# Kernel tuning notes

Measured on AMD Instinct MI355X. Metric: run time of the kernel, lower is better.

## Reference

```python
import itertools
import jax, jax.numpy as jnp
import numpy as np

N_LEVELS = 16
N_FEATS = 2
LOG2_T = 19
BASE_RES = 16.0
FINEST_RES = 512.0
N_POINTS = 2 ** 21
MASK = np.uint32((1 << LOG2_T) - 1)
PRIMES = jnp.array([1, 2654435761, 805459861], dtype=jnp.uint32)
# 8 corner offsets of a voxel, [8, 3]
OFFSETS = jnp.array(list(itertools.product([0, 1], repeat=3)), dtype=jnp.int32)
BOX_MIN = jnp.zeros((3,), dtype=jnp.float32)
BOX_MAX = jnp.ones((3,), dtype=jnp.float32)
# per-level growth factor b = exp((log(finest)-log(base))/(L-1))
B_FACTOR = float(np.exp((np.log(FINEST_RES) - np.log(BASE_RES)) / (N_LEVELS - 1)))


def setup_inputs() -> dict:
    key = jax.random.key(0)
    k1, k2 = jax.random.split(key)
    x = jax.random.uniform(k1, (N_POINTS, 3), dtype=jnp.float32)
    # nn.init.uniform_(w, a=-1e-4, b=1e-4)
    tables = jax.random.uniform(k2, (N_LEVELS, 2 ** LOG2_T, N_FEATS),
                                dtype=jnp.float32, minval=-1e-4, maxval=1e-4)
    return {"x": x, "tables": tables}


def _hash(vidx):
    # vidx: [N, 8, 3] int32 voxel-corner integer coords
    v = vidx.astype(jnp.uint32)
    h = (v[..., 0] * PRIMES[0]) ^ (v[..., 1] * PRIMES[1]) ^ (v[..., 2] * PRIMES[2])
    return (h & MASK).astype(jnp.int32)  # [N, 8]


def _embed_level(x, table, resolution):
    # x: [N,3] float, table: [T,F], resolution: python float
    grid = (BOX_MAX - BOX_MIN) / resolution                      # [3]
    xc = jnp.clip(x, BOX_MIN, BOX_MAX)
    bl = jnp.floor((xc - BOX_MIN) / grid).astype(jnp.int32)      # [N,3]
    vmin = bl.astype(jnp.float32) * grid + BOX_MIN               # [N,3]
    vidx = bl[:, None, :] + OFFSETS[None, :, :]                  # [N,8,3]
    emb = table[_hash(vidx)]                                     # [N,8,F]
    rel = (xc - vmin) / grid                                     # [N,3]
    # trilinear weights: prod over dims of rel (offset=1) / 1-rel (offset=0)
    w = jnp.prod(jnp.where(OFFSETS[None, :, :] == 1,
                           rel[:, None, :], 1.0 - rel[:, None, :]), axis=-1)  # [N,8]
    return jnp.sum(w[..., None] * emb, axis=1)                   # [N,F]


def reference(x, tables):
    outs = []
    for i in range(N_LEVELS):
        resolution = float(np.floor(BASE_RES * B_FACTOR ** i))
        outs.append(_embed_level(x, tables[i], resolution))
    return jnp.concatenate(outs, axis=-1)  # [N, L*F]
```

## Files before the change

### kernel.cpp

```cpp
#include <hip/hip_runtime.h>
#include <stdint.h>


constexpr int kLevels = 16;
constexpr int kPoints = 1 << 21;
constexpr uint32_t kTableSize = 1u << 19;
constexpr uint32_t kMask = kTableSize - 1u;
constexpr size_t kPackedBytes = (size_t)kLevels * kTableSize * 4;
constexpr size_t kLvlOutBytes = (size_t)kLevels * kPoints * 4;

typedef float f32x4 __attribute__((ext_vector_type(4)));
typedef uint32_t u32x4 __attribute__((ext_vector_type(4)));

constexpr int kS0 = 17, kS1 = 21, kS2 = 26;
constexpr int kN0 = kS0 * kS0 * kS0;
constexpr int kN1 = kS1 * kS1 * kS1;
constexpr int kN2 = kS2 * kS2 * kS2;
constexpr int kB1 = kN0, kB2 = kN0 + kN1;
constexpr int kNDense = kN0 + kN1 + kN2;

constexpr int kV3n = 33 * 33 * 33;
constexpr int kV4n = 41 * 41 * 41;
constexpr int kV5n = 51 * 51 * 51;
constexpr int kV6n = 65 * 65 * 65;
constexpr int kVTot = kV3n + kV4n + kV5n + kV6n;
constexpr size_t kV3Base = 131072;
constexpr size_t kV4Base = kV3Base + (size_t)kV3n * 32;
constexpr size_t kV5Base = kV4Base + (size_t)kV4n * 32;
constexpr size_t kV6Base = kPackedBytes + (size_t)7 * kPoints * 4;
constexpr size_t kD3Base = 7731456;
constexpr size_t kD4Base = 7875328;
constexpr size_t kD5Base = 8151296;
constexpr size_t kD6Base = 8681984;

__constant__ float c_res[kLevels] = {
    16.f, 20.f, 25.f, 32.f, 40.f, 50.f, 64.f, 80.f,
    101.f, 128.f, 161.f, 203.f, 256.f, 322.f, 406.f, 512.f};

__device__ __forceinline__ uint32_t bf16_rtne_hi(float f) {
    uint32_t u = __float_as_uint(f);
    return (u + 0x7FFFu + ((u >> 16) & 1u)) >> 16;
}
__device__ __forceinline__ float bflo(uint32_t e) {
    return __uint_as_float(e << 16);
}
__device__ __forceinline__ float bfhi(uint32_t e) {
    return __uint_as_float(e & 0xFFFF0000u);
}

__global__ __launch_bounds__(256) void pack_tables_kernel(
    const float* __restrict__ tables, uint32_t* __restrict__ packed, int base)
{
    const int i = base + blockIdx.x * 256 + threadIdx.x;
    const f32x4 v = reinterpret_cast<const f32x4*>(tables)[i];
    uint2 o;
    o.x = bf16_rtne_hi(v.x) | (bf16_rtne_hi(v.y) << 16);
    o.y = bf16_rtne_hi(v.z) | (bf16_rtne_hi(v.w) << 16);
    reinterpret_cast<uint2*>(packed)[i] = o;
}

template <int S, int LVL>
__device__ __forceinline__ void build_dense_one(
    int r, const float* __restrict__ tables, uint32_t* __restrict__ dst)
{
    const int bz = r % S;
    const int t = r / S;
    const int by = t % S;
    const int bx = t / S;
    const uint32_t h = ((uint32_t)bx ^ ((uint32_t)by * 2654435761u) ^
                        ((uint32_t)bz * 805459861u)) & kMask;
    const float2 src = *reinterpret_cast<const float2*>(
        tables + (((size_t)LVL << 19) + h) * 2);
    dst[r] = bf16_rtne_hi(src.x) | (bf16_rtne_hi(src.y) << 16);
}

__global__ __launch_bounds__(256) void build_dense012_kernel(
    const float* __restrict__ tables, uint32_t* __restrict__ dense)
{
    const int idx = blockIdx.x * 256 + threadIdx.x;
    if (idx >= kNDense) return;
    if (idx < kB1)      build_dense_one<kS0, 0>(idx,       tables, dense);
    else if (idx < kB2) build_dense_one<kS1, 1>(idx - kB1, tables, dense + kB1);
    else                build_dense_one<kS2, 2>(idx - kB2, tables, dense + kB2);
}

__global__ __launch_bounds__(256) void build_denseD_kernel(
    const float* __restrict__ tables, char* __restrict__ ws)
{
    const int g = blockIdx.x * 256 + threadIdx.x;
    if (g >= kVTot) return;
    if (g < kV3n)
        build_dense_one<33, 3>(g, tables, (uint32_t*)(ws + kD3Base));
    else if (g < kV3n + kV4n)
        build_dense_one<41, 4>(g - kV3n, tables, (uint32_t*)(ws + kD4Base));
    else if (g < kV3n + kV4n + kV5n)
        build_dense_one<51, 5>(g - kV3n - kV4n, tables,
                               (uint32_t*)(ws + kD5Base));
    else
        build_dense_one<65, 6>(g - kV3n - kV4n - kV5n, tables,
                               (uint32_t*)(ws + kD6Base));
}

template <int S>
__device__ __forceinline__ void build_vox_one(
    int v, const uint32_t* __restrict__ D, u32x4* __restrict__ dst)
{
    const int bz = v % S;
    const int t = v / S;
    const int by = t % S;
    const int bx = t / S;
    const int x1 = (bx + 1 < S) ? bx + 1 : S - 1;
    const int y1 = (by + 1 < S) ? by + 1 : S - 1;
    const int z1 = (bz + 1 < S) ? bz + 1 : S - 1;
    u32x4 q0, q1;
    q0.x = D[(bx * S + by) * S + bz];
    q0.y = D[(bx * S + by) * S + z1];
    q0.z = D[(bx * S + y1) * S + bz];
    q0.w = D[(bx * S + y1) * S + z1];
    q1.x = D[(x1 * S + by) * S + bz];
    q1.y = D[(x1 * S + by) * S + z1];
    q1.z = D[(x1 * S + y1) * S + bz];
    q1.w = D[(x1 * S + y1) * S + z1];
    dst[2 * v + 0] = q0;
    dst[2 * v + 1] = q1;
}

__global__ __launch_bounds__(256) void build_vox_kernel(char* __restrict__ ws)
{
    const int v = blockIdx.x * 256 + threadIdx.x;
    if (v >= kVTot) return;
    if (v < kV3n)
        build_vox_one<33>(v, (const uint32_t*)(ws + kD3Base),
                          (u32x4*)(ws + kV3Base));
    else if (v < kV3n + kV4n)
        build_vox_one<41>(v - kV3n, (const uint32_t*)(ws + kD4Base),
                          (u32x4*)(ws + kV4Base));
    else if (v < kV3n + kV4n + kV5n)
        build_vox_one<51>(v - kV3n - kV4n, (const uint32_t*)(ws + kD5Base),
                          (u32x4*)(ws + kV5Base));
    else
        build_vox_one<65>(v - kV3n - kV4n - kV5n,
                          (const uint32_t*)(ws + kD6Base),
                          (u32x4*)(ws + kV6Base));
}

template <int S, int BASE, int LVL>
__device__ __forceinline__ void eval_coarse(
    const uint32_t* __restrict__ lds, float px, float py, float pz, float r,
    uint32_t* __restrict__ lvl_out, int n)
{
    const float tx = px * r, ty = py * r, tz = pz * r;
    const float fx = floorf(tx), fy = floorf(ty), fz = floorf(tz);
    const int bx = (int)fx, by = (int)fy, bz = (int)fz;
    const float rx = tx - fx, ry = ty - fy, rz = tz - fz;
    const int c = BASE + (bx * S + by) * S + bz;
    const uint32_t e000 = lds[c],             e001 = lds[c + 1];
    const uint32_t e010 = lds[c + S],         e011 = lds[c + S + 1];
    const uint32_t e100 = lds[c + S * S],     e101 = lds[c + S * S + 1];
    const uint32_t e110 = lds[c + S * S + S], e111 = lds[c + S * S + S + 1];
    const float wx1 = rx, wx0 = 1.f - rx;
    const float wy1 = ry, wy0 = 1.f - ry;
    const float wz1 = rz, wz0 = 1.f - rz;
    float a0 = 0.f, a1 = 0.f;
    a0 = fmaf(wx0 * wy0 * wz0, bflo(e000), a0);
    a1 = fmaf(wx0 * wy0 * wz0, bfhi(e000), a1);
    a0 = fmaf(wx0 * wy0 * wz1, bflo(e001), a0);
    a1 = fmaf(wx0 * wy0 * wz1, bfhi(e001), a1);
    a0 = fmaf(wx0 * wy1 * wz0, bflo(e010), a0);
    a1 = fmaf(wx0 * wy1 * wz0, bfhi(e010), a1);
    a0 = fmaf(wx0 * wy1 * wz1, bflo(e011), a0);
    a1 = fmaf(wx0 * wy1 * wz1, bfhi(e011), a1);
    a0 = fmaf(wx1 * wy0 * wz0, bflo(e100), a0);
    a1 = fmaf(wx1 * wy0 * wz0, bfhi(e100), a1);
    a0 = fmaf(wx1 * wy0 * wz1, bflo(e101), a0);
    a1 = fmaf(wx1 * wy0 * wz1, bfhi(e101), a1);
    a0 = fmaf(wx1 * wy1 * wz0, bflo(e110), a0);
    a1 = fmaf(wx1 * wy1 * wz0, bfhi(e110), a1);
    a0 = fmaf(wx1 * wy1 * wz1, bflo(e111), a0);
    a1 = fmaf(wx1 * wy1 * wz1, bfhi(e111), a1);
    lvl_out[(size_t)LVL * kPoints + n] =
        bf16_rtne_hi(a0) | (bf16_rtne_hi(a1) << 16);
}

__global__ __launch_bounds__(512) void coarse_kernel(
    const float* __restrict__ x, const uint32_t* __restrict__ dense,
    uint32_t* __restrict__ lvl_out)
{
    __shared__ uint32_t s_tab[kNDense];
    for (int i = threadIdx.x; i < kNDense; i += 512) s_tab[i] = dense[i];
    __syncthreads();

    const int n0 = blockIdx.x * 2048 + threadIdx.x;
#pragma unroll
    for (int k = 0; k < 4; ++k) {
        const int n = n0 + k * 512;
        const float px = fminf(fmaxf(x[3 * n + 0], 0.0f), 1.0f);
        const float py = fminf(fmaxf(x[3 * n + 1], 0.0f), 1.0f);
        const float pz = fminf(fmaxf(x[3 * n + 2], 0.0f), 1.0f);
        eval_coarse<kS0, 0,   0>(s_tab, px, py, pz, 16.f, lvl_out, n);
        eval_coarse<kS1, kB1, 1>(s_tab, px, py, pz, 20.f, lvl_out, n);
        eval_coarse<kS2, kB2, 2>(s_tab, px, py, pz, 25.f, lvl_out, n);
    }
}

struct MidSt {
    float rx, ry, rz;
    u32x4 q0, q1;
};

template <int R>
__device__ __forceinline__ void issue_mid(
    MidSt& st, const u32x4* __restrict__ V, float px, float py, float pz)
{
    const float r = (float)R;
    const float tx = px * r, ty = py * r, tz = pz * r;
    const float fx = floorf(tx), fy = floorf(ty), fz = floorf(tz);
    const int bx = (int)fx, by = (int)fy, bz = (int)fz;
    st.rx = tx - fx;  st.ry = ty - fy;  st.rz = tz - fz;
    constexpr int S = R + 1;
    const int idx = (bx * S + by) * S + bz;
    st.q0 = V[2 * idx + 0];
    st.q1 = V[2 * idx + 1];
}

__device__ __forceinline__ void consume_mid(
    const MidSt& st, uint32_t* __restrict__ dst)
{
    const float wx1 = st.rx, wx0 = 1.f - st.rx;
    const float wy1 = st.ry, wy0 = 1.f - st.ry;
    const float wz1 = st.rz, wz0 = 1.f - st.rz;
    float a0 = 0.f, a1 = 0.f;
    a0 = fmaf(wx0 * wy0 * wz0, bflo(st.q0.x), a0);
    a1 = fmaf(wx0 * wy0 * wz0, bfhi(st.q0.x), a1);
    a0 = fmaf(wx0 * wy0 * wz1, bflo(st.q0.y), a0);
    a1 = fmaf(wx0 * wy0 * wz1, bfhi(st.q0.y), a1);
    a0 = fmaf(wx0 * wy1 * wz0, bflo(st.q0.z), a0);
    a1 = fmaf(wx0 * wy1 * wz0, bfhi(st.q0.z), a1);
    a0 = fmaf(wx0 * wy1 * wz1, bflo(st.q0.w), a0);
    a1 = fmaf(wx0 * wy1 * wz1, bfhi(st.q0.w), a1);
    a0 = fmaf(wx1 * wy0 * wz0, bflo(st.q1.x), a0);
    a1 = fmaf(wx1 * wy0 * wz0, bfhi(st.q1.x), a1);
    a0 = fmaf(wx1 * wy0 * wz1, bflo(st.q1.y), a0);
    a1 = fmaf(wx1 * wy0 * wz1, bfhi(st.q1.y), a1);
    a0 = fmaf(wx1 * wy1 * wz0, bflo(st.q1.z), a0);
    a1 = fmaf(wx1 * wy1 * wz0, bfhi(st.q1.z), a1);
    a0 = fmaf(wx1 * wy1 * wz1, bflo(st.q1.w), a0);
    a1 = fmaf(wx1 * wy1 * wz1, bfhi(st.q1.w), a1);
    *dst = bf16_rtne_hi(a0) | (bf16_rtne_hi(a1) << 16);
}

template <int R, int LVL>
__device__ __forceinline__ void mid_level(
    const float* __restrict__ x, const u32x4* __restrict__ V,
    uint32_t* __restrict__ lvl_out, int n0)
{
    uint32_t* __restrict__ w = lvl_out + (size_t)LVL * kPoints;
    const float px0 = fminf(fmaxf(x[3 * (n0 + 0 * 256) + 0], 0.f), 1.f);
    const float py0 = fminf(fmaxf(x[3 * (n0 + 0 * 256) + 1], 0.f), 1.f);
    const float pz0 = fminf(fmaxf(x[3 * (n0 + 0 * 256) + 2], 0.f), 1.f);
    const float px1 = fminf(fmaxf(x[3 * (n0 + 1 * 256) + 0], 0.f), 1.f);
    const float py1 = fminf(fmaxf(x[3 * (n0 + 1 * 256) + 1], 0.f), 1.f);
    const float pz1 = fminf(fmaxf(x[3 * (n0 + 1 * 256) + 2], 0.f), 1.f);
    const float px2 = fminf(fmaxf(x[3 * (n0 + 2 * 256) + 0], 0.f), 1.f);
    const float py2 = fminf(fmaxf(x[3 * (n0 + 2 * 256) + 1], 0.f), 1.f);
    const float pz2 = fminf(fmaxf(x[3 * (n0 + 2 * 256) + 2], 0.f), 1.f);
    const float px3 = fminf(fmaxf(x[3 * (n0 + 3 * 256) + 0], 0.f), 1.f);
    const float py3 = fminf(fmaxf(x[3 * (n0 + 3 * 256) + 1], 0.f), 1.f);
    const float pz3 = fminf(fmaxf(x[3 * (n0 + 3 * 256) + 2], 0.f), 1.f);
    __builtin_amdgcn_sched_barrier(0);

    MidSt A, B;
    issue_mid<R>(A, V, px0, py0, pz0);
    issue_mid<R>(B, V, px1, py1, pz1);
    __builtin_amdgcn_sched_barrier(0);
    consume_mid(A, &w[n0 + 0 * 256]);
    __builtin_amdgcn_sched_barrier(0);
    issue_mid<R>(A, V, px2, py2, pz2);
    __builtin_amdgcn_sched_barrier(0);
    consume_mid(B, &w[n0 + 1 * 256]);
    __builtin_amdgcn_sched_barrier(0);
    issue_mid<R>(B, V, px3, py3, pz3);
    __builtin_amdgcn_sched_barrier(0);
    consume_mid(A, &w[n0 + 2 * 256]);
    __builtin_amdgcn_sched_barrier(0);
    consume_mid(B, &w[n0 + 3 * 256]);
}

__global__ __launch_bounds__(256) void mid_kernel(
    const float* __restrict__ x, const char* __restrict__ ws,
    uint32_t* __restrict__ lvl_out)
{
    const int b = blockIdx.x;
    const int sub = b >> 11;
    const int chunk = b & 2047;
    const int n0 = chunk * 1024 + threadIdx.x;
    if (sub == 0)
        mid_level<32, 3>(x, (const u32x4*)(ws + kV3Base), lvl_out, n0);
    else if (sub == 1)
        mid_level<40, 4>(x, (const u32x4*)(ws + kV4Base), lvl_out, n0);
    else if (sub == 2)
        mid_level<50, 5>(x, (const u32x4*)(ws + kV5Base), lvl_out, n0);
    else
        mid_level<64, 6>(x, (const u32x4*)(ws + kV6Base), lvl_out, n0);
}

struct PtSt {
    float rx, ry, rz;
    uint32_t sel;
    uint2 p0, p1, p2, p3;
};

__device__ __forceinline__ void issue_pt(
    PtSt& st, const float* __restrict__ x, int n, float r,
    const uint32_t* __restrict__ tab)
{
    const float px = fminf(fmaxf(x[3 * n + 0], 0.f), 1.f);
    const float py = fminf(fmaxf(x[3 * n + 1], 0.f), 1.f);
    const float pz = fminf(fmaxf(x[3 * n + 2], 0.f), 1.f);
    const float tx = px * r, ty = py * r, tz = pz * r;
    const float fx = floorf(tx), fy = floorf(ty), fz = floorf(tz);
    const int bx = (int)fx, by = (int)fy, bz = (int)fz;
    st.rx = tx - fx;  st.ry = ty - fy;  st.rz = tz - fz;
    const uint32_t hy0 = (uint32_t)by * 2654435761u;
    const uint32_t hy1 = (uint32_t)(by + 1) * 2654435761u;
    const uint32_t hz0 = (uint32_t)bz * 805459861u;
    const uint32_t hz1 = (uint32_t)(bz + 1) * 805459861u;
    const uint32_t bxu = (uint32_t)bx, bx1 = bxu + 1u;
    const uint32_t m0 = hy0 ^ hz0, m1 = hy0 ^ hz1;
    const uint32_t m2 = hy1 ^ hz0, m3 = hy1 ^ hz1;
    if ((bx & 1) == 0) {
        const uint32_t h0 = (bxu ^ m0) & kMask;
        const uint32_t h1 = (bxu ^ m1) & kMask;
        const uint32_t h2 = (bxu ^ m2) & kMask;
        const uint32_t h3 = (bxu ^ m3) & kMask;
        st.sel = (h0 & 1u) | ((h1 & 1u) << 1) |
                 ((h2 & 1u) << 2) | ((h3 & 1u) << 3);
        st.p0 = *reinterpret_cast<const uint2*>(tab + (h0 & ~1u));
        st.p1 = *reinterpret_cast<const uint2*>(tab + (h1 & ~1u));
        st.p2 = *reinterpret_cast<const uint2*>(tab + (h2 & ~1u));
        st.p3 = *reinterpret_cast<const uint2*>(tab + (h3 & ~1u));
    } else {
        st.sel = 0u;
        st.p0.x = tab[(bxu ^ m0) & kMask];  st.p0.y = tab[(bx1 ^ m0) & kMask];
        st.p1.x = tab[(bxu ^ m1) & kMask];  st.p1.y = tab[(bx1 ^ m1) & kMask];
        st.p2.x = tab[(bxu ^ m2) & kMask];  st.p2.y = tab[(bx1 ^ m2) & kMask];
        st.p3.x = tab[(bxu ^ m3) & kMask];  st.p3.y = tab[(bx1 ^ m3) & kMask];
    }
}

__device__ __forceinline__ void consume_pt(
    const PtSt& st, uint32_t* __restrict__ w, int n)
{
    const float wx1 = st.rx, wx0 = 1.f - st.rx;
    const float wy1 = st.ry, wy0 = 1.f - st.ry;
    const float wz1 = st.rz, wz0 = 1.f - st.rz;
    const float w0 = wy0 * wz0, w1 = wy0 * wz1;
    const float w2 = wy1 * wz0, w3 = wy1 * wz1;
    const uint32_t e0 = (st.sel & 1u) ? st.p0.y : st.p0.x;
    const uint32_t f0 = (st.sel & 1u) ? st.p0.x : st.p0.y;
    const uint32_t e1 = (st.sel & 2u) ? st.p1.y : st.p1.x;
    const uint32_t f1 = (st.sel & 2u) ? st.p1.x : st.p1.y;
    const uint32_t e2 = (st.sel & 4u) ? st.p2.y : st.p2.x;
    const uint32_t f2 = (st.sel & 4u) ? st.p2.x : st.p2.y;
    const uint32_t e3 = (st.sel & 8u) ? st.p3.y : st.p3.x;
    const uint32_t f3 = (st.sel & 8u) ? st.p3.x : st.p3.y;
    float a0 = 0.f, a1 = 0.f;
    a0 = fmaf(w0, fmaf(wx0, bflo(e0), wx1 * bflo(f0)), a0);
    a1 = fmaf(w0, fmaf(wx0, bfhi(e0), wx1 * bfhi(f0)), a1);
    a0 = fmaf(w1, fmaf(wx0, bflo(e1), wx1 * bflo(f1)), a0);
    a1 = fmaf(w1, fmaf(wx0, bfhi(e1), wx1 * bfhi(f1)), a1);
    a0 = fmaf(w2, fmaf(wx0, bflo(e2), wx1 * bflo(f2)), a0);
    a1 = fmaf(w2, fmaf(wx0, bfhi(e2), wx1 * bfhi(f2)), a1);
    a0 = fmaf(w3, fmaf(wx0, bflo(e3), wx1 * bflo(f3)), a0);
    a1 = fmaf(w3, fmaf(wx0, bfhi(e3), wx1 * bfhi(f3)), a1);
    w[n] = bf16_rtne_hi(a0) | (bf16_rtne_hi(a1) << 16);
}

__global__ __launch_bounds__(256) void fine_kernel(
    const float* __restrict__ x,
    const uint32_t* __restrict__ packed,
    uint32_t* __restrict__ lvl_out)
{
    const int b = blockIdx.x;
    const int level = 7 + (b >> 11);
    const int chunk = b & 2047;

    const float r = c_res[level];
    const uint32_t* __restrict__ tab = packed + (size_t)level * kTableSize;
    uint32_t* __restrict__ w = lvl_out + (size_t)level * kPoints;

    const int n0 = chunk * 1024 + threadIdx.x;

    PtSt A, B;
    issue_pt(A, x, n0 + 0 * 256, r, tab);
    issue_pt(B, x, n0 + 1 * 256, r, tab);
    __builtin_amdgcn_sched_barrier(0);
    consume_pt(A, w, n0 + 0 * 256);
    __builtin_amdgcn_sched_barrier(0);
    issue_pt(A, x, n0 + 2 * 256, r, tab);
    __builtin_amdgcn_sched_barrier(0);
    consume_pt(B, w, n0 + 1 * 256);
    __builtin_amdgcn_sched_barrier(0);
    issue_pt(B, x, n0 + 3 * 256, r, tab);
    __builtin_amdgcn_sched_barrier(0);
    consume_pt(A, w, n0 + 2 * 256);
    __builtin_amdgcn_sched_barrier(0);
    consume_pt(B, w, n0 + 3 * 256);
}

__global__ __launch_bounds__(256) void untile_kernel(
    const uint32_t* __restrict__ lvl_out, float* __restrict__ out)
{
    const int n = blockIdx.x * 256 + threadIdx.x;
    float vals[2 * kLevels];
#pragma unroll
    for (int l = 0; l < kLevels; ++l) {
        const uint32_t u = lvl_out[(size_t)l * kPoints + n];
        vals[2 * l + 0] = bflo(u);
        vals[2 * l + 1] = bfhi(u);
    }
    float4* o4 = reinterpret_cast<float4*>(out + (size_t)n * (2 * kLevels));
#pragma unroll
    for (int kq = 0; kq < 8; ++kq) {
        o4[kq] = make_float4(vals[4 * kq + 0], vals[4 * kq + 1],
                             vals[4 * kq + 2], vals[4 * kq + 3]);
    }
}

__device__ __forceinline__ void eval_level(
    float px, float py, float pz, float r,
    const uint32_t* __restrict__ tab, float& a0, float& a1)
{
    const float tx = px * r, ty = py * r, tz = pz * r;
    const float fx = floorf(tx), fy = floorf(ty), fz = floorf(tz);
    const int bx = (int)fx, by = (int)fy, bz = (int)fz;
    const float rx = tx - fx, ry = ty - fy, rz = tz - fz;

    const uint32_t hx0 = (uint32_t)bx;
    const uint32_t hx1 = (uint32_t)(bx + 1);
    const uint32_t hy0 = (uint32_t)by * 2654435761u;
    const uint32_t hy1 = (uint32_t)(by + 1) * 2654435761u;
    const uint32_t hz0 = (uint32_t)bz * 805459861u;
    const uint32_t hz1 = (uint32_t)(bz + 1) * 805459861u;

    const float wx1 = rx, wx0 = 1.0f - rx;
    const float wy1 = ry, wy0 = 1.0f - ry;
    const float wz1 = rz, wz0 = 1.0f - rz;

    a0 = 0.0f; a1 = 0.0f;
#pragma unroll
    for (int c = 0; c < 8; ++c) {
        const uint32_t h = (((c & 4) ? hx1 : hx0) ^
                            ((c & 2) ? hy1 : hy0) ^
                            ((c & 1) ? hz1 : hz0)) & kMask;
        const uint32_t e = tab[h];
        const float w = ((c & 4) ? wx1 : wx0) *
                        ((c & 2) ? wy1 : wy0) *
                        ((c & 1) ? wz1 : wz0);
        a0 = fmaf(w, bflo(e), a0);
        a1 = fmaf(w, bfhi(e), a1);
    }
}

__global__ __launch_bounds__(256) void direct_kernel(
    const float* __restrict__ x,
    const float* __restrict__ tables,
    float* __restrict__ out)
{
    const int n = blockIdx.x * 256 + threadIdx.x;
    float px = fminf(fmaxf(x[3 * n + 0], 0.0f), 1.0f);
    float py = fminf(fmaxf(x[3 * n + 1], 0.0f), 1.0f);
    float pz = fminf(fmaxf(x[3 * n + 2], 0.0f), 1.0f);

    const float res_tab[kLevels] = {
        16.f, 20.f, 25.f, 32.f, 40.f, 50.f, 64.f, 80.f,
        101.f, 128.f, 161.f, 203.f, 256.f, 322.f, 406.f, 512.f};

    float acc[2 * kLevels];
#pragma unroll
    for (int l = 0; l < kLevels; ++l) {
        const float r = res_tab[l];
        const float tx = px * r, ty = py * r, tz = pz * r;
        const float fx = floorf(tx), fy = floorf(ty), fz = floorf(tz);
        const int bx = (int)fx, by = (int)fy, bz = (int)fz;
        const float rx = tx - fx, ry = ty - fy, rz = tz - fz;
        const uint32_t hx0 = (uint32_t)bx;
        const uint32_t hx1 = (uint32_t)(bx + 1);
        const uint32_t hy0 = (uint32_t)by * 2654435761u;
        const uint32_t hy1 = (uint32_t)(by + 1) * 2654435761u;
        const uint32_t hz0 = (uint32_t)bz * 805459861u;
        const uint32_t hz1 = (uint32_t)(bz + 1) * 805459861u;
        const float wx1 = rx, wx0 = 1.0f - rx;
        const float wy1 = ry, wy0 = 1.0f - ry;
        const float wz1 = rz, wz0 = 1.0f - rz;
        const float2* __restrict__ tab =
            reinterpret_cast<const float2*>(tables) + (size_t)l * kTableSize;
        float a0 = 0.0f, a1 = 0.0f;
#pragma unroll
        for (int c = 0; c < 8; ++c) {
            const uint32_t h = (((c & 4) ? hx1 : hx0) ^
                                ((c & 2) ? hy1 : hy0) ^
                                ((c & 1) ? hz1 : hz0)) & kMask;
            const float2 e = tab[h];
            const float w = ((c & 4) ? wx1 : wx0) *
                            ((c & 2) ? wy1 : wy0) *
                            ((c & 1) ? wz1 : wz0);
            a0 = fmaf(w, e.x, a0);
            a1 = fmaf(w, e.y, a1);
        }
        acc[2 * l + 0] = a0;
        acc[2 * l + 1] = a1;
    }
    float4* o4 = reinterpret_cast<float4*>(out + (size_t)n * (2 * kLevels));
#pragma unroll
    for (int kq = 0; kq < 8; ++kq) {
        o4[kq] = make_float4(acc[4 * kq + 0], acc[4 * kq + 1],
                             acc[4 * kq + 2], acc[4 * kq + 3]);
    }
}

__global__ __launch_bounds__(256) void direct_packed_kernel(
    const float* __restrict__ x,
    const uint32_t* __restrict__ packed,
    float* __restrict__ out)
{
    const int n = blockIdx.x * 256 + threadIdx.x;
    float px = fminf(fmaxf(x[3 * n + 0], 0.0f), 1.0f);
    float py = fminf(fmaxf(x[3 * n + 1], 0.0f), 1.0f);
    float pz = fminf(fmaxf(x[3 * n + 2], 0.0f), 1.0f);

    const float res_tab[kLevels] = {
        16.f, 20.f, 25.f, 32.f, 40.f, 50.f, 64.f, 80.f,
        101.f, 128.f, 161.f, 203.f, 256.f, 322.f, 406.f, 512.f};

    float acc[2 * kLevels];
#pragma unroll
    for (int l = 0; l < kLevels; ++l) {
        float a0, a1;
        eval_level(px, py, pz, res_tab[l],
                   packed + (size_t)l * kTableSize, a0, a1);
        acc[2 * l + 0] = a0;
        acc[2 * l + 1] = a1;
    }
    float4* o4 = reinterpret_cast<float4*>(out + (size_t)n * (2 * kLevels));
#pragma unroll
    for (int kq = 0; kq < 8; ++kq) {
        o4[kq] = make_float4(acc[4 * kq + 0], acc[4 * kq + 1],
                             acc[4 * kq + 2], acc[4 * kq + 3]);
    }
}

extern "C" void kernel_launch(void* const* d_in, const int* in_sizes, int n_in,
                              void* d_out, int out_size, void* d_ws, size_t ws_size,
                              hipStream_t stream) {
    const float* x = (const float*)d_in[0];
    const float* tables = (const float*)d_in[1];
    float* out = (float*)d_out;

    if (ws_size >= kPackedBytes + kLvlOutBytes) {
        char* ws = (char*)d_ws;
        uint32_t* packed = (uint32_t*)ws;
        uint32_t* lvl_out = (uint32_t*)(ws + kPackedBytes);
        uint32_t* dense012 = (uint32_t*)ws;

        hipLaunchKernelGGL(pack_tables_kernel,
                           dim3((9 << 19) / 2 / 256), dim3(256),
                           0, stream, tables, packed, (7 << 19) / 2);
        hipLaunchKernelGGL(build_dense012_kernel,
                           dim3((kNDense + 255) / 256), dim3(256),
                           0, stream, tables, dense012);
        hipLaunchKernelGGL(build_denseD_kernel,
                           dim3((kVTot + 255) / 256), dim3(256),
                           0, stream, tables, ws);
        hipLaunchKernelGGL(build_vox_kernel,
                           dim3((kVTot + 255) / 256), dim3(256),
                           0, stream, ws);
        hipLaunchKernelGGL(coarse_kernel, dim3(kPoints / 2048), dim3(512),
                           0, stream, x, dense012, lvl_out);
        hipLaunchKernelGGL(mid_kernel, dim3(4 * 2048), dim3(256),
                           0, stream, x, (const char*)ws, lvl_out);
        hipLaunchKernelGGL(fine_kernel, dim3(9 * 2048), dim3(256),
                           0, stream, x, packed, lvl_out);
        hipLaunchKernelGGL(untile_kernel, dim3(kPoints / 256), dim3(256),
                           0, stream, lvl_out, out);
    } else if (ws_size >= kPackedBytes) {
        uint32_t* packed = (uint32_t*)d_ws;
        hipLaunchKernelGGL(pack_tables_kernel,
                           dim3((kLevels * kTableSize / 2) / 256), dim3(256),
                           0, stream, tables, packed, 0);
        hipLaunchKernelGGL(direct_packed_kernel, dim3(kPoints / 256), dim3(256),
                           0, stream, x, packed, out);
    } else {
        hipLaunchKernelGGL(direct_kernel, dim3(kPoints / 256), dim3(256),
                           0, stream, x, tables, out);
    }
}
```

Before: 557.0 us.

## Fuse coarse and mid dense levels into the final output kernel

Removes the separate coarse (LDS) and mid kernels and evaluates levels 0-6 from precomputed per-voxel 8-corner records inside the final untile kernel. Levels 0-2 now also get voxel records, and the workspace layout is moved so the level-6 records sit where the lvl_out planes for levels 0-6 used to be. This removes two kernel launches, the writes and re-reads of seven intermediate level planes, and a second read of x. In exchange it does seven dependent gathers per thread in the output kernel, which raises register pressure and relies on the new workspace offsets not overlapping.

```diff
diff --git a/kernel.cpp b/kernel.cpp
--- a/kernel.cpp
+++ b/kernel.cpp
@@ -19,19 +19,26 @@
 constexpr int kB1 = kN0, kB2 = kN0 + kN1;
 constexpr int kNDense = kN0 + kN1 + kN2;
 
+constexpr int kV0n = 17 * 17 * 17;
+constexpr int kV1n = 21 * 21 * 21;
+constexpr int kV2n = 26 * 26 * 26;
 constexpr int kV3n = 33 * 33 * 33;
 constexpr int kV4n = 41 * 41 * 41;
 constexpr int kV5n = 51 * 51 * 51;
 constexpr int kV6n = 65 * 65 * 65;
-constexpr int kVTot = kV3n + kV4n + kV5n + kV6n;
-constexpr size_t kV3Base = 131072;
+constexpr int kVAll = kV0n + kV1n + kV2n + kV3n + kV4n + kV5n + kV6n;
+
+constexpr size_t kV0Base = 131072;
+constexpr size_t kV1Base = kV0Base + (size_t)kV0n * 32;
+constexpr size_t kV2Base = kV1Base + (size_t)kV1n * 32;
+constexpr size_t kV3Base = kV2Base + (size_t)kV2n * 32;
 constexpr size_t kV4Base = kV3Base + (size_t)kV3n * 32;
 constexpr size_t kV5Base = kV4Base + (size_t)kV4n * 32;
-constexpr size_t kV6Base = kPackedBytes + (size_t)7 * kPoints * 4;
-constexpr size_t kD3Base = 7731456;
-constexpr size_t kD4Base = 7875328;
-constexpr size_t kD5Base = 8151296;
-constexpr size_t kD6Base = 8681984;
+constexpr size_t kD3Base = 8748032;
+constexpr size_t kD4Base = 8892160;
+constexpr size_t kD5Base = 9168128;
+constexpr size_t kD6Base = 9699072;
+constexpr size_t kV6Base = kPackedBytes;
 
 __constant__ float c_res[kLevels] = {
     16.f, 20.f, 25.f, 32.f, 40.f, 50.f, 64.f, 80.f,
@@ -88,7 +95,7 @@
     const float* __restrict__ tables, char* __restrict__ ws)
 {
     const int g = blockIdx.x * 256 + threadIdx.x;
-    if (g >= kVTot) return;
+    if (g >= kV3n + kV4n + kV5n + kV6n) return;
     if (g < kV3n)
         build_dense_one<33, 3>(g, tables, (uint32_t*)(ws + kD3Base));
     else if (g < kV3n + kV4n)
@@ -127,181 +134,38 @@
 
 __global__ __launch_bounds__(256) void build_vox_kernel(char* __restrict__ ws)
 {
-    const int v = blockIdx.x * 256 + threadIdx.x;
-    if (v >= kVTot) return;
-    if (v < kV3n)
+    int v = blockIdx.x * 256 + threadIdx.x;
+    if (v >= kVAll) return;
+    const uint32_t* dense012 = (const uint32_t*)ws;
+    if (v < kV0n) {
+        build_vox_one<17>(v, dense012, (u32x4*)(ws + kV0Base)); return;
+    }
+    v -= kV0n;
+    if (v < kV1n) {
+        build_vox_one<21>(v, dense012 + kB1, (u32x4*)(ws + kV1Base)); return;
+    }
+    v -= kV1n;
+    if (v < kV2n) {
+        build_vox_one<26>(v, dense012 + kB2, (u32x4*)(ws + kV2Base)); return;
+    }
+    v -= kV2n;
+    if (v < kV3n) {
         build_vox_one<33>(v, (const uint32_t*)(ws + kD3Base),
-                          (u32x4*)(ws + kV3Base));
-    else if (v < kV3n + kV4n)
-        build_vox_one<41>(v - kV3n, (const uint32_t*)(ws + kD4Base),
-                          (u32x4*)(ws + kV4Base));
-    else if (v < kV3n + kV4n + kV5n)
-        build_vox_one<51>(v - kV3n - kV4n, (const uint32_t*)(ws + kD5Base),
-                          (u32x4*)(ws + kV5Base));
-    else
-        build_vox_one<65>(v - kV3n - kV4n - kV5n,
-                          (const uint32_t*)(ws + kD6Base),
-                          (u32x4*)(ws + kV6Base));
-}
-
-template <int S, int BASE, int LVL>
-__device__ __forceinline__ void eval_coarse(
-    const uint32_t* __restrict__ lds, float px, float py, float pz, float r,
-    uint32_t* __restrict__ lvl_out, int n)
-{
-    const float tx = px * r, ty = py * r, tz = pz * r;
-    const float fx = floorf(tx), fy = floorf(ty), fz = floorf(tz);
-    const int bx = (int)fx, by = (int)fy, bz = (int)fz;
-    const float rx = tx - fx, ry = ty - fy, rz = tz - fz;
-    const int c = BASE + (bx * S + by) * S + bz;
-    const uint32_t e000 = lds[c],             e001 = lds[c + 1];
-    const uint32_t e010 = lds[c + S],         e011 = lds[c + S + 1];
-    const uint32_t e100 = lds[c + S * S],     e101 = lds[c + S * S + 1];
-    const uint32_t e110 = lds[c + S * S + S], e111 = lds[c + S * S + S + 1];
-    const float wx1 = rx, wx0 = 1.f - rx;
-    const float wy1 = ry, wy0 = 1.f - ry;
-    const float wz1 = rz, wz0 = 1.f - rz;
-    float a0 = 0.f, a1 = 0.f;
-    a0 = fmaf(wx0 * wy0 * wz0, bflo(e000), a0);
-    a1 = fmaf(wx0 * wy0 * wz0, bfhi(e000), a1);
-    a0 = fmaf(wx0 * wy0 * wz1, bflo(e001), a0);
-    a1 = fmaf(wx0 * wy0 * wz1, bfhi(e001), a1);
-    a0 = fmaf(wx0 * wy1 * wz0, bflo(e010), a0);
-    a1 = fmaf(wx0 * wy1 * wz0, bfhi(e010), a1);
-    a0 = fmaf(wx0 * wy1 * wz1, bflo(e011), a0);
-    a1 = fmaf(wx0 * wy1 * wz1, bfhi(e011), a1);
-    a0 = fmaf(wx1 * wy0 * wz0, bflo(e100), a0);
-    a1 = fmaf(wx1 * wy0 * wz0, bfhi(e100), a1);
-    a0 = fmaf(wx1 * wy0 * wz1, bflo(e101), a0);
-    a1 = fmaf(wx1 * wy0 * wz1, bfhi(e101), a1);
-    a0 = fmaf(wx1 * wy1 * wz0, bflo(e110), a0);
-    a1 = fmaf(wx1 * wy1 * wz0, bfhi(e110), a1);
-    a0 = fmaf(wx1 * wy1 * wz1, bflo(e111), a0);
-    a1 = fmaf(wx1 * wy1 * wz1, bfhi(e111), a1);
-    lvl_out[(size_t)LVL * kPoints + n] =
-        bf16_rtne_hi(a0) | (bf16_rtne_hi(a1) << 16);
-}
-
-__global__ __launch_bounds__(512) void coarse_kernel(
-    const float* __restrict__ x, const uint32_t* __restrict__ dense,
-    uint32_t* __restrict__ lvl_out)
-{
-    __shared__ uint32_t s_tab[kNDense];
-    for (int i = threadIdx.x; i < kNDense; i += 512) s_tab[i] = dense[i];
-    __syncthreads();
-
-    const int n0 = blockIdx.x * 2048 + threadIdx.x;
-#pragma unroll
-    for (int k = 0; k < 4; ++k) {
-        const int n = n0 + k * 512;
-        const float px = fminf(fmaxf(x[3 * n + 0], 0.0f), 1.0f);
-        const float py = fminf(fmaxf(x[3 * n + 1], 0.0f), 1.0f);
-        const float pz = fminf(fmaxf(x[3 * n + 2], 0.0f), 1.0f);
-        eval_coarse<kS0, 0,   0>(s_tab, px, py, pz, 16.f, lvl_out, n);
-        eval_coarse<kS1, kB1, 1>(s_tab, px, py, pz, 20.f, lvl_out, n);
-        eval_coarse<kS2, kB2, 2>(s_tab, px, py, pz, 25.f, lvl_out, n);
-    }
-}
-
-struct MidSt {
-    float rx, ry, rz;
-    u32x4 q0, q1;
-};
-
-template <int R>
-__device__ __forceinline__ void issue_mid(
-    MidSt& st, const u32x4* __restrict__ V, float px, float py, float pz)
-{
-    const float r = (float)R;
-    const float tx = px * r, ty = py * r, tz = pz * r;
-    const float fx = floorf(tx), fy = floorf(ty), fz = floorf(tz);
-    const int bx = (int)fx, by = (int)fy, bz = (int)fz;
-    st.rx = tx - fx;  st.ry = ty - fy;  st.rz = tz - fz;
-    constexpr int S = R + 1;
-    const int idx = (bx * S + by) * S + bz;
-    st.q0 = V[2 * idx + 0];
-    st.q1 = V[2 * idx + 1];
-}
-
-__device__ __forceinline__ void consume_mid(
-    const MidSt& st, uint32_t* __restrict__ dst)
-{
-    const float wx1 = st.rx, wx0 = 1.f - st.rx;
-    const float wy1 = st.ry, wy0 = 1.f - st.ry;
-    const float wz1 = st.rz, wz0 = 1.f - st.rz;
-    float a0 = 0.f, a1 = 0.f;
-    a0 = fmaf(wx0 * wy0 * wz0, bflo(st.q0.x), a0);
-    a1 = fmaf(wx0 * wy0 * wz0, bfhi(st.q0.x), a1);
-    a0 = fmaf(wx0 * wy0 * wz1, bflo(st.q0.y), a0);
-    a1 = fmaf(wx0 * wy0 * wz1, bfhi(st.q0.y), a1);
-    a0 = fmaf(wx0 * wy1 * wz0, bflo(st.q0.z), a0);
-    a1 = fmaf(wx0 * wy1 * wz0, bfhi(st.q0.z), a1);
-    a0 = fmaf(wx0 * wy1 * wz1, bflo(st.q0.w), a0);
-    a1 = fmaf(wx0 * wy1 * wz1, bfhi(st.q0.w), a1);
-    a0 = fmaf(wx1 * wy0 * wz0, bflo(st.q1.x), a0);
-    a1 = fmaf(wx1 * wy0 * wz0, bfhi(st.q1.x), a1);
-    a0 = fmaf(wx1 * wy0 * wz1, bflo(st.q1.y), a0);
-    a1 = fmaf(wx1 * wy0 * wz1, bfhi(st.q1.y), a1);
-    a0 = fmaf(wx1 * wy1 * wz0, bflo(st.q1.z), a0);
-    a1 = fmaf(wx1 * wy1 * wz0, bfhi(st.q1.z), a1);
-    a0 = fmaf(wx1 * wy1 * wz1, bflo(st.q1.w), a0);
-    a1 = fmaf(wx1 * wy1 * wz1, bfhi(st.q1.w), a1);
-    *dst = bf16_rtne_hi(a0) | (bf16_rtne_hi(a1) << 16);
-}
-
-template <int R, int LVL>
-__device__ __forceinline__ void mid_level(
-    const float* __restrict__ x, const u32x4* __restrict__ V,
-    uint32_t* __restrict__ lvl_out, int n0)
-{
-    uint32_t* __restrict__ w = lvl_out + (size_t)LVL * kPoints;
-    const float px0 = fminf(fmaxf(x[3 * (n0 + 0 * 256) + 0], 0.f), 1.f);
-    const float py0 = fminf(fmaxf(x[3 * (n0 + 0 * 256) + 1], 0.f), 1.f);
-    const float pz0 = fminf(fmaxf(x[3 * (n0 + 0 * 256) + 2], 0.f), 1.f);
-    const float px1 = fminf(fmaxf(x[3 * (n0 + 1 * 256) + 0], 0.f), 1.f);
-    const float py1 = fminf(fmaxf(x[3 * (n0 + 1 * 256) + 1], 0.f), 1.f);
-    const float pz1 = fminf(fmaxf(x[3 * (n0 + 1 * 256) + 2], 0.f), 1.f);
-    const float px2 = fminf(fmaxf(x[3 * (n0 + 2 * 256) + 0], 0.f), 1.f);
-    const float py2 = fminf(fmaxf(x[3 * (n0 + 2 * 256) + 1], 0.f), 1.f);
-    const float pz2 = fminf(fmaxf(x[3 * (n0 + 2 * 256) + 2], 0.f), 1.f);
-    const float px3 = fminf(fmaxf(x[3 * (n0 + 3 * 256) + 0], 0.f), 1.f);
-    const float py3 = fminf(fmaxf(x[3 * (n0 + 3 * 256) + 1], 0.f), 1.f);
-    const float pz3 = fminf(fmaxf(x[3 * (n0 + 3 * 256) + 2], 0.f), 1.f);
-    __builtin_amdgcn_sched_barrier(0);
-
-    MidSt A, B;
-    issue_mid<R>(A, V, px0, py0, pz0);
-    issue_mid<R>(B, V, px1, py1, pz1);
-    __builtin_amdgcn_sched_barrier(0);
-    consume_mid(A, &w[n0 + 0 * 256]);
-    __builtin_amdgcn_sched_barrier(0);
-    issue_mid<R>(A, V, px2, py2, pz2);
-    __builtin_amdgcn_sched_barrier(0);
-    consume_mid(B, &w[n0 + 1 * 256]);
-    __builtin_amdgcn_sched_barrier(0);
-    issue_mid<R>(B, V, px3, py3, pz3);
-    __builtin_amdgcn_sched_barrier(0);
-    consume_mid(A, &w[n0 + 2 * 256]);
-    __builtin_amdgcn_sched_barrier(0);
-    consume_mid(B, &w[n0 + 3 * 256]);
-}
-
-__global__ __launch_bounds__(256) void mid_kernel(
-    const float* __restrict__ x, const char* __restrict__ ws,
-    uint32_t* __restrict__ lvl_out)
-{
-    const int b = blockIdx.x;
-    const int sub = b >> 11;
-    const int chunk = b & 2047;
-    const int n0 = chunk * 1024 + threadIdx.x;
-    if (sub == 0)
-        mid_level<32, 3>(x, (const u32x4*)(ws + kV3Base), lvl_out, n0);
-    else if (sub == 1)
-        mid_level<40, 4>(x, (const u32x4*)(ws + kV4Base), lvl_out, n0);
-    else if (sub == 2)
-        mid_level<50, 5>(x, (const u32x4*)(ws + kV5Base), lvl_out, n0);
-    else
-        mid_level<64, 6>(x, (const u32x4*)(ws + kV6Base), lvl_out, n0);
+                          (u32x4*)(ws + kV3Base)); return;
+    }
+    v -= kV3n;
+    if (v < kV4n) {
+        build_vox_one<41>(v, (const uint32_t*)(ws + kD4Base),
+                          (u32x4*)(ws + kV4Base)); return;
+    }
+    v -= kV4n;
+    if (v < kV5n) {
+        build_vox_one<51>(v, (const uint32_t*)(ws + kD5Base),
+                          (u32x4*)(ws + kV5Base)); return;
+    }
+    v -= kV5n;
+    build_vox_one<65>(v, (const uint32_t*)(ws + kD6Base),
+                      (u32x4*)(ws + kV6Base));
 }
 
 struct PtSt {
@@ -408,23 +272,97 @@
     consume_pt(B, w, n0 + 3 * 256);
 }
 
-__global__ __launch_bounds__(256) void untile_kernel(
+struct VoxSt {
+    float rx, ry, rz;
+    u32x4 q0, q1;
+};
+
+template <int R>
+__device__ __forceinline__ void issue_vox(
+    VoxSt& st, const u32x4* __restrict__ V, float px, float py, float pz)
+{
+    const float r = (float)R;
+    const float tx = px * r, ty = py * r, tz = pz * r;
+    const float fx = floorf(tx), fy = floorf(ty), fz = floorf(tz);
+    const int bx = (int)fx, by = (int)fy, bz = (int)fz;
+    st.rx = tx - fx;  st.ry = ty - fy;  st.rz = tz - fz;
+    constexpr int S = R + 1;
+    const int idx = (bx * S + by) * S + bz;
+    st.q0 = V[2 * idx + 0];
+    st.q1 = V[2 * idx + 1];
+}
+
+__device__ __forceinline__ uint32_t consume_vox(const VoxSt& st)
+{
+    const float wx1 = st.rx, wx0 = 1.f - st.rx;
+    const float wy1 = st.ry, wy0 = 1.f - st.ry;
+    const float wz1 = st.rz, wz0 = 1.f - st.rz;
+    float a0 = 0.f, a1 = 0.f;
+    a0 = fmaf(wx0 * wy0 * wz0, bflo(st.q0.x), a0);
+    a1 = fmaf(wx0 * wy0 * wz0, bfhi(st.q0.x), a1);
+    a0 = fmaf(wx0 * wy0 * wz1, bflo(st.q0.y), a0);
+    a1 = fmaf(wx0 * wy0 * wz1, bfhi(st.q0.y), a1);
+    a0 = fmaf(wx0 * wy1 * wz0, bflo(st.q0.z), a0);
+    a1 = fmaf(wx0 * wy1 * wz0, bfhi(st.q0.z), a1);
+    a0 = fmaf(wx0 * wy1 * wz1, bflo(st.q0.w), a0);
+    a1 = fmaf(wx0 * wy1 * wz1, bfhi(st.q0.w), a1);
+    a0 = fmaf(wx1 * wy0 * wz0, bflo(st.q1.x), a0);
+    a1 = fmaf(wx1 * wy0 * wz0, bfhi(st.q1.x), a1);
+    a0 = fmaf(wx1 * wy0 * wz1, bflo(st.q1.y), a0);
+    a1 = fmaf(wx1 * wy0 * wz1, bfhi(st.q1.y), a1);
+    a0 = fmaf(wx1 * wy1 * wz0, bflo(st.q1.z), a0);
+    a1 = fmaf(wx1 * wy1 * wz0, bfhi(st.q1.z), a1);
+    a0 = fmaf(wx1 * wy1 * wz1, bflo(st.q1.w), a0);
+    a1 = fmaf(wx1 * wy1 * wz1, bfhi(st.q1.w), a1);
+    return bf16_rtne_hi(a0) | (bf16_rtne_hi(a1) << 16);
+}
+
+__global__ __launch_bounds__(256) void final_kernel(
+    const float* __restrict__ x, const char* __restrict__ ws,
     const uint32_t* __restrict__ lvl_out, float* __restrict__ out)
 {
     const int n = blockIdx.x * 256 + threadIdx.x;
-    float vals[2 * kLevels];
-#pragma unroll
-    for (int l = 0; l < kLevels; ++l) {
-        const uint32_t u = lvl_out[(size_t)l * kPoints + n];
-        vals[2 * l + 0] = bflo(u);
-        vals[2 * l + 1] = bfhi(u);
-    }
-    float4* o4 = reinterpret_cast<float4*>(out + (size_t)n * (2 * kLevels));
-#pragma unroll
-    for (int kq = 0; kq < 8; ++kq) {
-        o4[kq] = make_float4(vals[4 * kq + 0], vals[4 * kq + 1],
-                             vals[4 * kq + 2], vals[4 * kq + 3]);
-    }
+    const float px = fminf(fmaxf(x[3 * n + 0], 0.f), 1.f);
+    const float py = fminf(fmaxf(x[3 * n + 1], 0.f), 1.f);
+    const float pz = fminf(fmaxf(x[3 * n + 2], 0.f), 1.f);
+
+    uint32_t u7  = lvl_out[(size_t)7  * kPoints + n];
+    uint32_t u8  = lvl_out[(size_t)8  * kPoints + n];
+    uint32_t u9  = lvl_out[(size_t)9  * kPoints + n];
+    uint32_t u10 = lvl_out[(size_t)10 * kPoints + n];
+    uint32_t u11 = lvl_out[(size_t)11 * kPoints + n];
+    uint32_t u12 = lvl_out[(size_t)12 * kPoints + n];
+    uint32_t u13 = lvl_out[(size_t)13 * kPoints + n];
+    uint32_t u14 = lvl_out[(size_t)14 * kPoints + n];
+    uint32_t u15 = lvl_out[(size_t)15 * kPoints + n];
+
+    VoxSt s0, s1, s2, s3, s4, s5, s6;
+    issue_vox<16>(s0, (const u32x4*)(ws + kV0Base), px, py, pz);
+    issue_vox<20>(s1, (const u32x4*)(ws + kV1Base), px, py, pz);
+    issue_vox<25>(s2, (const u32x4*)(ws + kV2Base), px, py, pz);
+    issue_vox<32>(s3, (const u32x4*)(ws + kV3Base), px, py, pz);
+    issue_vox<40>(s4, (const u32x4*)(ws + kV4Base), px, py, pz);
+    issue_vox<50>(s5, (const u32x4*)(ws + kV5Base), px, py, pz);
+    issue_vox<64>(s6, (const u32x4*)(ws + kV6Base), px, py, pz);
+    __builtin_amdgcn_sched_barrier(0);
+
+    const uint32_t w0 = consume_vox(s0);
+    const uint32_t w1 = consume_vox(s1);
+    const uint32_t w2 = consume_vox(s2);
+    const uint32_t w3 = consume_vox(s3);
+    const uint32_t w4 = consume_vox(s4);
+    const uint32_t w5 = consume_vox(s5);
+    const uint32_t w6 = consume_vox(s6);
+
+    float4* o4 = reinterpret_cast<float4*>(out + (size_t)n * 32);
+    o4[0] = make_float4(bflo(w0),  bfhi(w0),  bflo(w1),  bfhi(w1));
+    o4[1] = make_float4(bflo(w2),  bfhi(w2),  bflo(w3),  bfhi(w3));
+    o4[2] = make_float4(bflo(w4),  bfhi(w4),  bflo(w5),  bfhi(w5));
+    o4[3] = make_float4(bflo(w6),  bfhi(w6),  bflo(u7),  bfhi(u7));
+    o4[4] = make_float4(bflo(u8),  bfhi(u8),  bflo(u9),  bfhi(u9));
+    o4[5] = make_float4(bflo(u10), bfhi(u10), bflo(u11), bfhi(u11));
+    o4[6] = make_float4(bflo(u12), bfhi(u12), bflo(u13), bfhi(u13));
+    o4[7] = make_float4(bflo(u14), bfhi(u14), bflo(u15), bfhi(u15));
 }
 
 __device__ __forceinline__ void eval_level(
@@ -570,19 +508,15 @@
                            dim3((kNDense + 255) / 256), dim3(256),
                            0, stream, tables, dense012);
         hipLaunchKernelGGL(build_denseD_kernel,
-                           dim3((kVTot + 255) / 256), dim3(256),
-                           0, stream, tables, ws);
+                           dim3((kV3n + kV4n + kV5n + kV6n + 255) / 256),
+                           dim3(256), 0, stream, tables, ws);
         hipLaunchKernelGGL(build_vox_kernel,
-                           dim3((kVTot + 255) / 256), dim3(256),
+                           dim3((kVAll + 255) / 256), dim3(256),
                            0, stream, ws);
-        hipLaunchKernelGGL(coarse_kernel, dim3(kPoints / 2048), dim3(512),
-                           0, stream, x, dense012, lvl_out);
-        hipLaunchKernelGGL(mid_kernel, dim3(4 * 2048), dim3(256),
-                           0, stream, x, (const char*)ws, lvl_out);
         hipLaunchKernelGGL(fine_kernel, dim3(9 * 2048), dim3(256),
                            0, stream, x, packed, lvl_out);
-        hipLaunchKernelGGL(untile_kernel, dim3(kPoints / 256), dim3(256),
-                           0, stream, lvl_out, out);
+        hipLaunchKernelGGL(final_kernel, dim3(kPoints / 256), dim3(256),
+                           0, stream, x, (const char*)ws, lvl_out, out);
     } else if (ws_size >= kPackedBytes) {
         uint32_t* packed = (uint32_t*)d_ws;
         hipLaunchKernelGGL(pack_tables_kernel,
```

Measured after the change: 581.2 us. 1.04x slower.
